# Performance work log

Measured on AMD Instinct MI355X. Metric: run time of the kernel, lower is better.

## Reference

```python
import jax, jax.numpy as jnp
import numpy as np
from jax import lax

SEQ, BATCH, INPUT, HIDDEN = 2048, 32, 256, 256


def setup_inputs() -> dict:
    key = jax.random.key(0)
    k1, k2, k3 = jax.random.split(key, 3)
    scale = 1.0 / np.sqrt(HIDDEN)
    return {
        "input": jax.random.normal(k1, (SEQ, BATCH, INPUT), dtype=jnp.float32),
        "W_ih": jax.random.normal(k2, (3 * HIDDEN, INPUT), dtype=jnp.float32) * scale,
        "W_hh": jax.random.normal(k3, (3 * HIDDEN, HIDDEN), dtype=jnp.float32) * scale,
        "b_ih": jnp.zeros((3 * HIDDEN,), dtype=jnp.float32),
        "b_hh": jnp.zeros((3 * HIDDEN,), dtype=jnp.float32),
    }


def reference(input, W_ih, W_hh, b_ih, b_hh):
    """Single-layer unidirectional CustomGRU forward.

    Faithful to the torch module, including its quirk: the n-gate gets the
    W_hh_n @ h contribution twice (once un-gated via `gates`, once gated by r).
    Returns (output [S,B,H], h_n [1,B,H]).
    """
    H = W_hh.shape[0] // 3
    W_hn = W_hh[2 * H:]  # [H, H]
    # Precompute input projections for all timesteps (same math, batched GEMM).
    x_proj = jnp.einsum('sbi,gi->sbg', input, W_ih) + b_ih + b_hh  # [S,B,3H]

    def step(h, xp):
        gates = xp + h @ W_hh.T  # [B, 3H]
        r, z, n = jnp.split(gates, 3, axis=1)
        r = jax.nn.sigmoid(r)
        z = jax.nn.sigmoid(z)
        n = jnp.tanh(n + r * (h @ W_hn.T))
        h_new = (1.0 - z) * n + z * h
        return h_new, h_new

    h0 = jnp.zeros((input.shape[1], H), dtype=input.dtype)
    h_last, output = lax.scan(step, h0, x_proj)
    return output, h_last[None, :, :]
```

## Files before the change

### kernel.cpp

```cpp
#include <hip/hip_runtime.h>
#include <stdint.h>
#include <stddef.h>

#define S_LEN 2048
#define BATCH 32
#define NIN   256
#define NH    256
#define NG    768

typedef _Float16 half2_t __attribute__((ext_vector_type(2)));
typedef _Float16 half8_t __attribute__((ext_vector_type(8)));
typedef int      int16v  __attribute__((ext_vector_type(16)));

#if __has_builtin(__builtin_amdgcn_exp2f)
#define EXP2F(x) __builtin_amdgcn_exp2f(x)
#else
#define EXP2F(x) exp2f(x)
#endif

static __device__ __forceinline__ float fdot2(half2_t a, half2_t b, float c) {
  return __builtin_amdgcn_fdot2(a, b, c, false);
}
static __device__ __forceinline__ half2_t pack2(float lo, float hi) {
  half2_t r; r[0] = (_Float16)lo; r[1] = (_Float16)hi; return r;
}
static __device__ __forceinline__ float sigmoid_fast(float x) {
  float e = EXP2F(-1.44269504088896340736f * x);
  return 1.0f / (1.0f + e);
}
static __device__ __forceinline__ float tanh_fast(float x) {
  float e = EXP2F(2.88539008177792681472f * x);
  return 1.0f - 2.0f / (1.0f + e);
}

#define BH(x)    __builtin_bit_cast(half2_t, (x))
#define BW(W, e) __builtin_bit_cast(half2_t, (int)((W)[e]))

#define DOT16(W, i0) do {                                                     \
    int4 q0 = hls[(i0) + 0], q1 = hls[(i0) + 1];                              \
    int4 q2 = hls[(i0) + 2], q3 = hls[(i0) + 3];                              \
    a0 = fdot2(BH(q0.x), BW(W, 0),  a0); a1 = fdot2(BH(q0.y), BW(W, 1),  a1);\
    a2 = fdot2(BH(q0.z), BW(W, 2),  a2); a3 = fdot2(BH(q0.w), BW(W, 3),  a3);\
    a0 = fdot2(BH(q1.x), BW(W, 4),  a0); a1 = fdot2(BH(q1.y), BW(W, 5),  a1);\
    a2 = fdot2(BH(q1.z), BW(W, 6),  a2); a3 = fdot2(BH(q1.w), BW(W, 7),  a3);\
    a0 = fdot2(BH(q2.x), BW(W, 8),  a0); a1 = fdot2(BH(q2.y), BW(W, 9),  a1);\
    a2 = fdot2(BH(q2.z), BW(W, 10), a2); a3 = fdot2(BH(q2.w), BW(W, 11), a3);\
    a0 = fdot2(BH(q3.x), BW(W, 12), a0); a1 = fdot2(BH(q3.y), BW(W, 13), a1);\
    a2 = fdot2(BH(q3.z), BW(W, 14), a2); a3 = fdot2(BH(q3.w), BW(W, 15), a3);\
  } while (0)

#define LDW(W, o) do {                                                        \
    int4 q0 = wsrc[(o) + 0], q1 = wsrc[(o) + 1];                              \
    int4 q2 = wsrc[(o) + 2], q3 = wsrc[(o) + 3];                              \
    W = (int16v){q0.x, q0.y, q0.z, q0.w, q1.x, q1.y, q1.z, q1.w,              \
                 q2.x, q2.y, q2.z, q2.w, q3.x, q3.y, q3.z, q3.w};             \
  } while (0)

__global__ __launch_bounds__(256) void prep_in_kernel(const float* __restrict__ in,
                                                      _Float16* __restrict__ in16) {
  size_t v = (size_t)blockIdx.x * 256 + threadIdx.x;
  const float4* p4 = (const float4*)in;
  float4 a = p4[v * 2 + 0];
  float4 b = p4[v * 2 + 1];
  half8_t o;
  o[0] = (_Float16)a.x; o[1] = (_Float16)a.y; o[2] = (_Float16)a.z; o[3] = (_Float16)a.w;
  o[4] = (_Float16)b.x; o[5] = (_Float16)b.y; o[6] = (_Float16)b.z; o[7] = (_Float16)b.w;
  ((half8_t*)in16)[v] = o;
}

__global__ __launch_bounds__(256) void prep_w_kernel(const float* __restrict__ W_ih,
                                                     const float* __restrict__ W_hh,
                                                     const float* __restrict__ b_ih,
                                                     const float* __restrict__ b_hh,
                                                     half2_t* __restrict__ whh2g,
                                                     half2_t* __restrict__ wih2,
                                                     float* __restrict__ bias) {
  int idx = blockIdx.x * 256 + threadIdx.x;
  if (idx < 128 * NG) {
    int g = idx >> 7, kk = idx & 127;
    whh2g[idx] = pack2(W_hh[(size_t)g * NH + 2 * kk], W_hh[(size_t)g * NH + 2 * kk + 1]);
  } else if (idx < 2 * 128 * NG) {
    int i2 = idx - 128 * NG;
    int g = i2 >> 7, kk = i2 & 127;
    wih2[(size_t)g * 128 + kk] = pack2(W_ih[(size_t)g * NIN + 2 * kk], W_ih[(size_t)g * NIN + 2 * kk + 1]);
  } else if (idx < 2 * 128 * NG + NG) {
    int g = idx - 2 * 128 * NG;
    bias[g] = b_ih[g] + b_hh[g];
  }
}

__global__
__attribute__((amdgpu_flat_work_group_size(768, 768), amdgpu_waves_per_eu(3, 3)))
void xproj_kernel(const _Float16* __restrict__ in16,
                  const half2_t* __restrict__ wih2,
                  const float* __restrict__ bias,
                  float* __restrict__ xp_out) {
  __shared__ char occ_pad[86016];
  {
    unsigned lp = (unsigned)(uintptr_t)&occ_pad[0];
    asm volatile("" :: "v"(lp));
  }
  const int g = threadIdx.x;
  const int row0 = blockIdx.x * 64;
  const float bg = bias[g];

  int16v w0, w1, w2, w3, w4, w5, w6, w7;
  {
    const int4* wsrc = (const int4*)(wih2 + (size_t)g * 128);
    LDW(w0, 0);  LDW(w1, 4);  LDW(w2, 8);  LDW(w3, 12);
    LDW(w4, 16); LDW(w5, 20); LDW(w6, 24); LDW(w7, 28);
  }

  for (int r = 0; r < 64; ++r) {
    const int row = row0 + r;
    const int4* hls = (const int4*)(in16 + (size_t)row * NIN);
    float a0 = 0.f, a1 = 0.f, a2 = 0.f, a3 = 0.f;
    DOT16(w0, 0);  DOT16(w1, 4);  DOT16(w2, 8);  DOT16(w3, 12);
    DOT16(w4, 16); DOT16(w5, 20); DOT16(w6, 24); DOT16(w7, 28);
    xp_out[(size_t)row * NG + g] = (a0 + a1) + (a2 + a3) + bg;
  }
}

struct SMemG {
  int   hbuf_i[2][128];
  float mv[NG];
  char  pad[81920];
};
static_assert(sizeof(SMemG) == 86016, "LDS clamp size");

__global__
__attribute__((amdgpu_flat_work_group_size(768, 768), amdgpu_waves_per_eu(3, 3)))
void gru_kernel(const float* __restrict__ xp,
                const half2_t* __restrict__ whh2g,
                float* __restrict__ out) {
  const int b = blockIdx.x;
  const int g = threadIdx.x;

  int16v w0, w1, w2, w3, w4, w5, w6, w7;
  {
    const int4* wsrc = (const int4*)(whh2g + (size_t)g * 128);
    LDW(w0, 0);  LDW(w1, 4);  LDW(w2, 8);  LDW(w3, 12);
    LDW(w4, 16); LDW(w5, 20); LDW(w6, 24); LDW(w7, 28);
  }

  __shared__ SMemG sm;
  {
    unsigned lp = (unsigned)(uintptr_t)&sm.pad[0];
    asm volatile("" :: "v"(lp));
  }

  if (g < NH) ((_Float16*)sm.hbuf_i)[g] = (_Float16)0.f;

  const float* xq = xp + (size_t)b * NG + g;
  float xr_c = 0.f, xz_c = 0.f, xn_c = 0.f;
  if (g < NH) { xr_c = xq[0]; xz_c = xq[NH]; xn_c = xq[2 * NH]; }
  xq += (size_t)BATCH * NG;
  float* op = out + (size_t)b * NH + g;

  float h = 0.f;
  __syncthreads();

  for (int t = 0; t < S_LEN; ++t) {
    float xr_n = 0.f, xz_n = 0.f, xn_n = 0.f;
    if (g < NH) { xr_n = xq[0]; xz_n = xq[NH]; xn_n = xq[2 * NH]; }

    const int4* hls = ((const int4*)sm.hbuf_i) + ((t & 1) << 5);
    float a0 = 0.f, a1 = 0.f, a2 = 0.f, a3 = 0.f;
    DOT16(w0, 0);  DOT16(w1, 4);  DOT16(w2, 8);  DOT16(w3, 12);
    DOT16(w4, 16); DOT16(w5, 20); DOT16(w6, 24); DOT16(w7, 28);
    sm.mv[g] = (a0 + a1) + (a2 + a3);
    __syncthreads();

    if (g < NH) {
      float mvr = sm.mv[g], mvz = sm.mv[NH + g], mvn = sm.mv[2 * NH + g];
      float r = sigmoid_fast(xr_c + mvr);
      float z = sigmoid_fast(xz_c + mvz);
      float n = tanh_fast(xn_c + mvn + r * mvn);
      h = z * (h - n) + n;
      op[0] = h;
      ((_Float16*)sm.hbuf_i)[(((t + 1) & 1) << 8) + g] = (_Float16)h;
    }
    __syncthreads();

    xr_c = xr_n; xz_c = xz_n; xn_c = xn_n;
    xq += (size_t)BATCH * NG;
    op += (size_t)BATCH * NH;
  }

  if (g < NH) out[(size_t)S_LEN * BATCH * NH + (size_t)b * NH + g] = h;
}

extern "C" void kernel_launch(void* const* d_in, const int* in_sizes, int n_in,
                              void* d_out, int out_size, void* d_ws, size_t ws_size,
                              hipStream_t stream) {
  const float* input = (const float*)d_in[0];
  const float* W_ih  = (const float*)d_in[1];
  const float* W_hh  = (const float*)d_in[2];
  const float* b_ih  = (const float*)d_in[3];
  const float* b_hh  = (const float*)d_in[4];
  float* out = (float*)d_out;

  const size_t SB = (size_t)S_LEN * BATCH;
  const size_t xp_b   = SB * NG * 4;
  const size_t in16_b = SB * NIN * 2;
  const size_t w_b    = (size_t)128 * NG * 4;

  char* p = (char*)d_ws;
  float*    xp    = (float*)p;                p += xp_b;
  _Float16* in16  = (_Float16*)p;             p += in16_b;
  half2_t*  whh2g = (half2_t*)p;              p += w_b;
  half2_t*  wih2  = (half2_t*)p;              p += w_b;
  float*    bias  = (float*)p;

  prep_in_kernel<<<8192, 256, 0, stream>>>(input, in16);
  prep_w_kernel<<<(2 * 128 * NG + NG + 255) / 256, 256, 0, stream>>>(W_ih, W_hh, b_ih, b_hh,
                                                                     whh2g, wih2, bias);
  xproj_kernel<<<1024, 768, 0, stream>>>(in16, wih2, bias, xp);
  gru_kernel<<<BATCH, 768, 0, stream>>>(xp, whh2g, out);
  (void)out_size; (void)n_in; (void)in_sizes; (void)ws_size;
}
```

Before: 2.796 ms.

## Split GRU recurrent matvec across thread quads with DPP reductions and one barrier

The recurrent kernel now runs 512 threads per batch block. Each quad of threads owns two hidden units across all three gates, and each thread covers a 64-wide slice of h. Partial dot products are combined with DPP quad reductions instead of an LDS matrix-vector buffer, so the gate math runs redundantly in every lane and only one barrier is needed per timestep instead of two. Weights are repacked in the prep kernel to match the new layout. The h buffer is padded to avoid LDS bank conflicts. The cost is 192 weight registers per thread and redundant activation math.

```diff
diff --git a/kernel.cpp b/kernel.cpp
--- a/kernel.cpp
+++ b/kernel.cpp
@@ -31,6 +31,13 @@
 static __device__ __forceinline__ float tanh_fast(float x) {
   float e = EXP2F(2.88539008177792681472f * x);
   return 1.0f - 2.0f / (1.0f + e);
+}
+
+static __device__ __forceinline__ float quad_sum(float v) {
+  int y1 = __builtin_amdgcn_mov_dpp(__builtin_bit_cast(int, v), 0xB1, 0xF, 0xF, true);
+  float s = v + __builtin_bit_cast(float, y1);
+  int y2 = __builtin_amdgcn_mov_dpp(__builtin_bit_cast(int, s), 0x4E, 0xF, 0xF, true);
+  return s + __builtin_bit_cast(float, y2);
 }
 
 #define BH(x)    __builtin_bit_cast(half2_t, (x))
@@ -49,6 +56,21 @@
     a2 = fdot2(BH(q3.z), BW(W, 14), a2); a3 = fdot2(BH(q3.w), BW(W, 15), a3);\
   } while (0)
 
+#define DOT6(q, U0, U1, U2, U3, U4, U5, o) do {                               \
+    a0 = fdot2(BH(q.x), BW(U0,(o)+0), a0); a1 = fdot2(BH(q.x), BW(U1,(o)+0), a1);\
+    a2 = fdot2(BH(q.x), BW(U2,(o)+0), a2); a3 = fdot2(BH(q.x), BW(U3,(o)+0), a3);\
+    a4 = fdot2(BH(q.x), BW(U4,(o)+0), a4); a5 = fdot2(BH(q.x), BW(U5,(o)+0), a5);\
+    a0 = fdot2(BH(q.y), BW(U0,(o)+1), a0); a1 = fdot2(BH(q.y), BW(U1,(o)+1), a1);\
+    a2 = fdot2(BH(q.y), BW(U2,(o)+1), a2); a3 = fdot2(BH(q.y), BW(U3,(o)+1), a3);\
+    a4 = fdot2(BH(q.y), BW(U4,(o)+1), a4); a5 = fdot2(BH(q.y), BW(U5,(o)+1), a5);\
+    a0 = fdot2(BH(q.z), BW(U0,(o)+2), a0); a1 = fdot2(BH(q.z), BW(U1,(o)+2), a1);\
+    a2 = fdot2(BH(q.z), BW(U2,(o)+2), a2); a3 = fdot2(BH(q.z), BW(U3,(o)+2), a3);\
+    a4 = fdot2(BH(q.z), BW(U4,(o)+2), a4); a5 = fdot2(BH(q.z), BW(U5,(o)+2), a5);\
+    a0 = fdot2(BH(q.w), BW(U0,(o)+3), a0); a1 = fdot2(BH(q.w), BW(U1,(o)+3), a1);\
+    a2 = fdot2(BH(q.w), BW(U2,(o)+3), a2); a3 = fdot2(BH(q.w), BW(U3,(o)+3), a3);\
+    a4 = fdot2(BH(q.w), BW(U4,(o)+3), a4); a5 = fdot2(BH(q.w), BW(U5,(o)+3), a5);\
+  } while (0)
+
 #define LDW(W, o) do {                                                        \
     int4 q0 = wsrc[(o) + 0], q1 = wsrc[(o) + 1];                              \
     int4 q2 = wsrc[(o) + 2], q3 = wsrc[(o) + 3];                              \
@@ -72,13 +94,19 @@
                                                      const float* __restrict__ W_hh,
                                                      const float* __restrict__ b_ih,
                                                      const float* __restrict__ b_hh,
-                                                     half2_t* __restrict__ whh2g,
+                                                     half2_t* __restrict__ whh3,
                                                      half2_t* __restrict__ wih2,
                                                      float* __restrict__ bias) {
   int idx = blockIdx.x * 256 + threadIdx.x;
   if (idx < 128 * NG) {
-    int g = idx >> 7, kk = idx & 127;
-    whh2g[idx] = pack2(W_hh[(size_t)g * NH + 2 * kk], W_hh[(size_t)g * NH + 2 * kk + 1]);
+    int tid = idx / 192;
+    int r   = idx - tid * 192;
+    int d   = r >> 5, kk = r & 31;
+    int gate = d >> 1, jj = d & 1;
+    int c  = tid & 3, j1 = tid >> 2;
+    int row = gate * NH + 2 * j1 + jj;
+    int col = 64 * c + 2 * kk;
+    whh3[idx] = pack2(W_hh[(size_t)row * NH + col], W_hh[(size_t)row * NH + col + 1]);
   } else if (idx < 2 * 128 * NG) {
     int i2 = idx - 128 * NG;
     int g = i2 >> 7, kk = i2 & 127;
@@ -110,6 +138,8 @@
     LDW(w0, 0);  LDW(w1, 4);  LDW(w2, 8);  LDW(w3, 12);
     LDW(w4, 16); LDW(w5, 20); LDW(w6, 24); LDW(w7, 28);
   }
+  asm volatile("" : "+v"(w0), "+v"(w1), "+v"(w2), "+v"(w3),
+                    "+v"(w4), "+v"(w5), "+v"(w6), "+v"(w7));
 
   for (int r = 0; r < 64; ++r) {
     const int row = row0 + r;
@@ -121,73 +151,84 @@
   }
 }
 
-struct SMemG {
-  int   hbuf_i[2][128];
-  float mv[NG];
-  char  pad[81920];
-};
-static_assert(sizeof(SMemG) == 86016, "LDS clamp size");
-
 __global__
-__attribute__((amdgpu_flat_work_group_size(768, 768), amdgpu_waves_per_eu(3, 3)))
+__attribute__((amdgpu_flat_work_group_size(512, 512), amdgpu_waves_per_eu(2, 2)))
 void gru_kernel(const float* __restrict__ xp,
-                const half2_t* __restrict__ whh2g,
+                const half2_t* __restrict__ whh3,
                 float* __restrict__ out) {
-  const int b = blockIdx.x;
-  const int g = threadIdx.x;
-
-  int16v w0, w1, w2, w3, w4, w5, w6, w7;
+  const int b   = blockIdx.x;
+  const int tid = threadIdx.x;
+  const int c   = tid & 3;
+  const int j1  = tid >> 2;
+  const int jj  = c & 1;
+  const int jmine = 2 * j1 + jj;
+
+  int16v W0a, W0b, W1a, W1b, W2a, W2b, W3a, W3b, W4a, W4b, W5a, W5b;
   {
-    const int4* wsrc = (const int4*)(whh2g + (size_t)g * 128);
-    LDW(w0, 0);  LDW(w1, 4);  LDW(w2, 8);  LDW(w3, 12);
-    LDW(w4, 16); LDW(w5, 20); LDW(w6, 24); LDW(w7, 28);
-  }
-
-  __shared__ SMemG sm;
-  {
-    unsigned lp = (unsigned)(uintptr_t)&sm.pad[0];
-    asm volatile("" :: "v"(lp));
-  }
-
-  if (g < NH) ((_Float16*)sm.hbuf_i)[g] = (_Float16)0.f;
-
-  const float* xq = xp + (size_t)b * NG + g;
-  float xr_c = 0.f, xz_c = 0.f, xn_c = 0.f;
-  if (g < NH) { xr_c = xq[0]; xz_c = xq[NH]; xn_c = xq[2 * NH]; }
+    const int4* wsrc = (const int4*)(whh3 + (size_t)tid * 192);
+    LDW(W0a, 0);  LDW(W0b, 4);  LDW(W1a, 8);  LDW(W1b, 12);
+    LDW(W2a, 16); LDW(W2b, 20); LDW(W3a, 24); LDW(W3b, 28);
+    LDW(W4a, 32); LDW(W4b, 36); LDW(W5a, 40); LDW(W5b, 44);
+  }
+  asm volatile("" : "+v"(W0a), "+v"(W0b), "+v"(W1a), "+v"(W1b),
+                    "+v"(W2a), "+v"(W2b), "+v"(W3a), "+v"(W3b),
+                    "+v"(W4a), "+v"(W4b), "+v"(W5a), "+v"(W5b));
+
+  __shared__ __attribute__((aligned(16))) char smh[1152];
+  if (tid < 288) ((int*)smh)[tid] = 0;
+
+  const float* xq = xp + (size_t)b * NG + jmine;
+  float xr_c = xq[0], xz_c = xq[NH], xn_c = xq[2 * NH];
   xq += (size_t)BATCH * NG;
-  float* op = out + (size_t)b * NH + g;
+  float* op = out + (size_t)b * NH + jmine;
+
+  const int wofs = 144 * (jmine >> 6) + 2 * (jmine & 63);
 
   float h = 0.f;
   __syncthreads();
 
   for (int t = 0; t < S_LEN; ++t) {
-    float xr_n = 0.f, xz_n = 0.f, xn_n = 0.f;
-    if (g < NH) { xr_n = xq[0]; xz_n = xq[NH]; xn_n = xq[2 * NH]; }
-
-    const int4* hls = ((const int4*)sm.hbuf_i) + ((t & 1) << 5);
-    float a0 = 0.f, a1 = 0.f, a2 = 0.f, a3 = 0.f;
-    DOT16(w0, 0);  DOT16(w1, 4);  DOT16(w2, 8);  DOT16(w3, 12);
-    DOT16(w4, 16); DOT16(w5, 20); DOT16(w6, 24); DOT16(w7, 28);
-    sm.mv[g] = (a0 + a1) + (a2 + a3);
-    __syncthreads();
-
-    if (g < NH) {
-      float mvr = sm.mv[g], mvz = sm.mv[NH + g], mvn = sm.mv[2 * NH + g];
-      float r = sigmoid_fast(xr_c + mvr);
-      float z = sigmoid_fast(xz_c + mvz);
-      float n = tanh_fast(xn_c + mvn + r * mvn);
-      h = z * (h - n) + n;
+    float xr_n = xq[0], xz_n = xq[NH], xn_n = xq[2 * NH];
+
+    const char* hb = smh + (t & 1) * 576 + c * 144;
+    float a0 = 0.f, a1 = 0.f, a2 = 0.f, a3 = 0.f, a4 = 0.f, a5 = 0.f;
+    int4 q0 = *(const int4*)(hb +   0), q1 = *(const int4*)(hb +  16);
+    int4 q2 = *(const int4*)(hb +  32), q3 = *(const int4*)(hb +  48);
+    int4 q4 = *(const int4*)(hb +  64), q5 = *(const int4*)(hb +  80);
+    int4 q6 = *(const int4*)(hb +  96), q7 = *(const int4*)(hb + 112);
+    DOT6(q0, W0a, W1a, W2a, W3a, W4a, W5a, 0);
+    DOT6(q1, W0a, W1a, W2a, W3a, W4a, W5a, 4);
+    DOT6(q2, W0a, W1a, W2a, W3a, W4a, W5a, 8);
+    DOT6(q3, W0a, W1a, W2a, W3a, W4a, W5a, 12);
+    DOT6(q4, W0b, W1b, W2b, W3b, W4b, W5b, 0);
+    DOT6(q5, W0b, W1b, W2b, W3b, W4b, W5b, 4);
+    DOT6(q6, W0b, W1b, W2b, W3b, W4b, W5b, 8);
+    DOT6(q7, W0b, W1b, W2b, W3b, W4b, W5b, 12);
+
+    float s0 = quad_sum(a0), s1 = quad_sum(a1);
+    float s2 = quad_sum(a2), s3 = quad_sum(a3);
+    float s4 = quad_sum(a4), s5 = quad_sum(a5);
+    float mvr = jj ? s1 : s0;
+    float mvz = jj ? s3 : s2;
+    float mvn = jj ? s5 : s4;
+
+    float r = sigmoid_fast(xr_c + mvr);
+    float z = sigmoid_fast(xz_c + mvz);
+    float n = tanh_fast(xn_c + mvn + r * mvn);
+    h = z * (h - n) + n;
+
+    if (c < 2) {
       op[0] = h;
-      ((_Float16*)sm.hbuf_i)[(((t + 1) & 1) << 8) + g] = (_Float16)h;
+      *(_Float16*)(smh + (((t + 1) & 1) * 576) + wofs) = (_Float16)h;
     }
-    __syncthreads();
+    asm volatile("s_waitcnt lgkmcnt(0)\n\ts_barrier" ::: "memory");
 
     xr_c = xr_n; xz_c = xz_n; xn_c = xn_n;
     xq += (size_t)BATCH * NG;
     op += (size_t)BATCH * NH;
   }
 
-  if (g < NH) out[(size_t)S_LEN * BATCH * NH + (size_t)b * NH + g] = h;
+  if (c < 2) out[(size_t)S_LEN * BATCH * NH + (size_t)b * NH + jmine] = h;
 }
 
 extern "C" void kernel_launch(void* const* d_in, const int* in_sizes, int n_in,
@@ -208,14 +249,14 @@
   char* p = (char*)d_ws;
   float*    xp    = (float*)p;                p += xp_b;
   _Float16* in16  = (_Float16*)p;             p += in16_b;
-  half2_t*  whh2g = (half2_t*)p;              p += w_b;
+  half2_t*  whh3  = (half2_t*)p;              p += w_b;
   half2_t*  wih2  = (half2_t*)p;              p += w_b;
   float*    bias  = (float*)p;
 
   prep_in_kernel<<<8192, 256, 0, stream>>>(input, in16);
   prep_w_kernel<<<(2 * 128 * NG + NG + 255) / 256, 256, 0, stream>>>(W_ih, W_hh, b_ih, b_hh,
-                                                                     whh2g, wih2, bias);
+                                                                     whh3, wih2, bias);
   xproj_kernel<<<1024, 768, 0, stream>>>(in16, wih2, bias, xp);
-  gru_kernel<<<BATCH, 768, 0, stream>>>(xp, whh2g, out);
+  gru_kernel<<<BATCH, 512, 0, stream>>>(xp, whh3, out);
   (void)out_size; (void)n_in; (void)in_sizes; (void)ws_size;
 }
```

Result: faster. 2.621 ms (-6.3%).
